# Kernel optimization log

Measured on AMD Instinct MI355X. Metric: run time of the kernel, lower is better.

## Reference

```python
import math
import jax, jax.numpy as jnp
import numpy as np

HID = 8
QNUM = 22
NUM_A = 11
NUM_LAYER = 6


def _ln(x, g, b, eps=1e-5):
    m = jnp.mean(x, axis=-1, keepdims=True)
    v = jnp.mean((x - m) ** 2, axis=-1, keepdims=True)
    return (x - m) / jnp.sqrt(v + eps) * g + b


def _conv1d_s2(x, w):
    # x: [N, C, L], w: [O, I, K=2], stride 2, no padding, no bias
    return jax.lax.conv_general_dilated(x, w, (2,), 'VALID', dimension_numbers=('NCH', 'OIH', 'NCH'))


def _qembed(hf):
    # product state amplitudes of RY(hf_q)|0> per qubit: [cos(t/2), sin(t/2)], kron over qubits
    c = jnp.cos(hf / 2.0)
    s = jnp.sin(hf / 2.0)
    state = jnp.ones((1,), dtype=hf.dtype)
    for q in range(hf.shape[0]):
        state = jnp.kron(state, jnp.stack([c[q], s[q]]))
    return state  # [2^Q]


def setup_inputs() -> dict:
    key = jax.random.key(0)
    ks = jax.random.split(key, 32)
    ix_list = [2] * NUM_A  # 2 electrons per atom -> n_e = 22 (even, <= QNUM)
    pos_ix = np.concatenate([np.arange(n) for n in ix_list])
    atom_ix = np.concatenate([np.full(n, i) for i, n in enumerate(ix_list)])
    L = NUM_LAYER
    g = lambda i, shp, s=1.0: jax.random.normal(ks[i], shp, dtype=jnp.float32) * s
    return dict(
        pos_a=g(0, (NUM_A, 3), 3.0),
        ix_a=jnp.asarray(ix_list, dtype=jnp.int32),
        pos_ix=jnp.asarray(pos_ix, dtype=jnp.int32),
        atom_ix=jnp.asarray(atom_ix, dtype=jnp.int32),
        rpos_w=g(1, (10, 3), 1.0),
        emb_w=g(2, (HID, 4), 0.5),
        emb_b=jnp.zeros((HID,), jnp.float32),
        Wq=g(3, (L, HID, HID), 0.35), bq=jnp.zeros((L, HID), jnp.float32),
        Wk=g(4, (L, HID, HID), 0.35), bk=jnp.zeros((L, HID), jnp.float32),
        Wv=g(5, (L, HID, HID), 0.35), bv=jnp.zeros((L, HID), jnp.float32),
        Wo=g(6, (L, HID, HID), 0.35), bo=jnp.zeros((L, HID), jnp.float32),
        W1=g(7, (L, 4 * HID, HID), 0.35), b1=jnp.zeros((L, 4 * HID), jnp.float32),
        W2=g(8, (L, HID, 4 * HID), 0.18), b2=jnp.zeros((L, HID), jnp.float32),
        ln1_g=jnp.ones((L, HID), jnp.float32), ln1_b=jnp.zeros((L, HID), jnp.float32),
        ln2_g=jnp.ones((L, HID), jnp.float32), ln2_b=jnp.zeros((L, HID), jnp.float32),
        Wi=g(9, (2 * HID, HID), 0.35), bi=jnp.zeros((2 * HID,), jnp.float32),
        ni_g=jnp.ones((2 * HID,), jnp.float32), ni_b=jnp.zeros((2 * HID,), jnp.float32),
        conv_a_w=g(10, (2 * HID, 2 * HID, 2), 0.25),
        conv_e_w=g(11, (2 * HID, 2 * HID, 2), 0.25),
        Wout=g(12, (2 ** QNUM, 2 * HID), 0.05),
        bout=jnp.zeros((2 ** QNUM,), jnp.float32),
    )


def reference(pos_a, ix_a, pos_ix, atom_ix, rpos_w, emb_w, emb_b,
              Wq, bq, Wk, bk, Wv, bv, Wo, bo, W1, b1, W2, b2,
              ln1_g, ln1_b, ln2_g, ln2_b,
              Wi, bi, ni_g, ni_b, conv_a_w, conv_e_w, Wout, bout):
    n_e = pos_ix.shape[0]
    pos_e = rpos_w[pos_ix] + pos_a[atom_ix]                 # [n_e, 3]
    ae = pos_e[:, None, :] - pos_a[None, :, :]              # [n_e, A, 3]
    r_ae = jnp.linalg.norm(ae, axis=2, keepdims=True)       # [n_e, A, 1]
    seq = jnp.concatenate([ae, r_ae], axis=-1) @ emb_w.T + emb_b  # [n_e, A, HID]
    amp_proto = ix_a.astype(seq.dtype)[None, :, None]       # broadcast of expanded ix_a
    amp_ae = jnp.std(r_ae, ddof=1)
    bias_ae = jnp.mean(r_ae)
    scale = jnp.sqrt(jnp.asarray(HID, seq.dtype))
    for l in range(Wq.shape[0]):
        x = amp_proto * seq
        q = x @ Wq[l].T + bq[l]
        k = x @ Wk[l].T + bk[l]
        v = x @ Wv[l].T + bv[l]
        att = jax.nn.softmax(jnp.einsum('bqh,bkh->bqk', q, k) / scale, axis=-1)
        a = jnp.einsum('bqk,bkh->bqh', att, v) @ Wo[l].T + bo[l]
        x = _ln(x + a, ln1_g[l], ln1_b[l])
        f = jax.nn.relu(x @ W1[l].T + b1[l]) @ W2[l].T + b2[l]
        seq = _ln(x + f, ln2_g[l], ln2_b[l])
    # pseudo-inverse projection (detached in torch)
    ae_inv = jax.lax.stop_gradient(jnp.linalg.inv(emb_w.T @ emb_w) @ emb_w.T)  # [4, HID]
    r = jnp.einsum('h,bah->ba', ae_inv[-1], seq)[..., None]  # [n_e, A, 1]
    r = amp_ae * (r - jnp.mean(r)) / jnp.std(r, ddof=1) + bias_ae
    x = (jnp.exp(-r) * amp_proto * seq) @ Wi.T + bi          # [n_e, A, 2*HID]
    x = jnp.swapaxes(x, -2, -1)                              # [n_e, 2*HID, A]
    y = jnp.mean(x, axis=-1)                                 # [n_e, 2*HID]
    amp_r = jnp.mean(jnp.exp(-jnp.swapaxes(r, -2, -1)), axis=-1)  # [n_e, 1]
    pad = jnp.zeros((x.shape[0], x.shape[1], 1), x.dtype)
    n_iter_a = (x.shape[-1] + 1) // 2
    for _ in range(n_iter_a):
        x = _conv1d_s2(jnp.concatenate([x, pad], axis=-1), conv_a_w)
    x = (amp_r * _ln(y + x[..., 0], ni_g, ni_b)).T           # [2*HID, n_e]
    y = jnp.mean(x, axis=-1)                                 # [2*HID]
    amp_r2 = jnp.mean(amp_r.T, axis=-1)                      # [1]
    x = x[None]                                              # [1, 2*HID, n_e]
    pad = jnp.zeros((1, x.shape[1], 1), x.dtype)
    n_iter_e = (x.shape[-1] + 1) // 2
    for _ in range(n_iter_e):
        x = _conv1d_s2(jnp.concatenate([x, pad], axis=-1), conv_e_w)
    x = amp_r2 * _ln(y + x[0, :, 0], ni_g, ni_b)             # [2*HID]
    psi = x @ Wout.T + bout                                  # [2^QNUM]
    hf = jnp.asarray(([math.pi, 0.0] * (n_e // 2)) + [0.0] * (QNUM - n_e), dtype=psi.dtype)
    bos = _qembed(hf)
    return psi + bos * (2.0 ** (QNUM / 2))
```

## Files before the change

kernel.cpp:

```cpp
#include <hip/hip_runtime.h>
#include <math.h>

#define NE 22
#define NA 11
#define HD 8
#define H2 16
#define QN 22
#define NL 6
#define CPAD 12
#define CSTR 17

struct QCS { float c[QN]; float s[QN]; };

#define RL(v, l) __uint_as_float(__builtin_amdgcn_readlane(__float_as_uint(v), (l)))

__device__ __forceinline__ float block_reduce_sum(float v, float* red, int tid) {
  red[tid] = v;
  __syncthreads();
  for (int off = 128; off > 0; off >>= 1) {
    if (tid < off) red[tid] += red[tid + off];
    __syncthreads();
  }
  float s = red[0];
  __syncthreads();
  return s;
}

__device__ __forceinline__ void ln_vec(const float* x, int n, const float* __restrict__ g,
                                       const float* __restrict__ bb, float* o) {
  float m = 0.f;
  for (int i = 0; i < n; i++) m += x[i];
  m /= (float)n;
  float v = 0.f;
  for (int i = 0; i < n; i++) { float d = x[i] - m; v += d * d; }
  v /= (float)n;
  float is = 1.0f / sqrtf(v + 1e-5f);
  for (int i = 0; i < n; i++) o[i] = (x[i] - m) * is * g[i] + bb[i];
}

__global__ __launch_bounds__(128, 1) void layers_kernel(
    const float* __restrict__ pos_a, const int* __restrict__ ix_a,
    const int* __restrict__ pos_ix, const int* __restrict__ atom_ix,
    const float* __restrict__ rpos_w, const float* __restrict__ emb_w,
    const float* __restrict__ emb_b,
    const float* __restrict__ Wq, const float* __restrict__ bq,
    const float* __restrict__ Wk, const float* __restrict__ bk,
    const float* __restrict__ Wv, const float* __restrict__ bv,
    const float* __restrict__ Wo, const float* __restrict__ bo,
    const float* __restrict__ W1, const float* __restrict__ b1,
    const float* __restrict__ W2, const float* __restrict__ b2,
    const float* __restrict__ ln1_g, const float* __restrict__ ln1_b,
    const float* __restrict__ ln2_g, const float* __restrict__ ln2_b,
    float* __restrict__ seq_out, float* __restrict__ rae_out)
{
  const int e = blockIdx.x;
  const int tid = threadIdx.x;
  const int a = tid >> 3;
  const int h = tid & 7;
  const bool act = (a < NA);

  __shared__ __align__(16) float sseq[NA][HD];
  __shared__ __align__(16) float sx[NA][HD];
  __shared__ __align__(16) float sq_[NA][HD];
  __shared__ __align__(16) float sk_[NA][HD];
  __shared__ __align__(16) float sv_[NA][HD];
  __shared__ __align__(16) float sav[NA][HD];
  __shared__ float ss[NA][12];
  __shared__ __align__(16) float sh_[NA][32];

  float amp_a = 0.f;
  if (act) {
    amp_a = (float)ix_a[a];
    int p = pos_ix[e], am = atom_ix[e];
    float d0 = rpos_w[p*3+0] + pos_a[am*3+0] - pos_a[a*3+0];
    float d1 = rpos_w[p*3+1] + pos_a[am*3+1] - pos_a[a*3+1];
    float d2 = rpos_w[p*3+2] + pos_a[am*3+2] - pos_a[a*3+2];
    float rae = sqrtf(d0*d0 + d1*d1 + d2*d2);
    float s = emb_b[h] + d0*emb_w[h*4+0] + d1*emb_w[h*4+1]
            + d2*emb_w[h*4+2] + rae*emb_w[h*4+3];
    sseq[a][h] = s;
    if (h == 0) rae_out[e*NA + a] = rae;
  }
  __syncthreads();

  const float iscale = 0.35355339059327373f;
  for (int l = 0; l < NL; l++) {
    float wq[8], wk[8], wv[8], wo[8], w1v[4][8], w2v[32];
    {
      const float4* q4 = (const float4*)(Wq + l*64 + h*8);
      float4 t0 = q4[0], t1 = q4[1];
      wq[0]=t0.x; wq[1]=t0.y; wq[2]=t0.z; wq[3]=t0.w; wq[4]=t1.x; wq[5]=t1.y; wq[6]=t1.z; wq[7]=t1.w;
      const float4* k4 = (const float4*)(Wk + l*64 + h*8);
      t0 = k4[0]; t1 = k4[1];
      wk[0]=t0.x; wk[1]=t0.y; wk[2]=t0.z; wk[3]=t0.w; wk[4]=t1.x; wk[5]=t1.y; wk[6]=t1.z; wk[7]=t1.w;
      const float4* v4 = (const float4*)(Wv + l*64 + h*8);
      t0 = v4[0]; t1 = v4[1];
      wv[0]=t0.x; wv[1]=t0.y; wv[2]=t0.z; wv[3]=t0.w; wv[4]=t1.x; wv[5]=t1.y; wv[6]=t1.z; wv[7]=t1.w;
      const float4* o4 = (const float4*)(Wo + l*64 + h*8);
      t0 = o4[0]; t1 = o4[1];
      wo[0]=t0.x; wo[1]=t0.y; wo[2]=t0.z; wo[3]=t0.w; wo[4]=t1.x; wo[5]=t1.y; wo[6]=t1.z; wo[7]=t1.w;
      #pragma unroll
      for (int j = 0; j < 4; j++) {
        const float4* w14 = (const float4*)(W1 + l*256 + (j*8 + h)*8);
        float4 u0 = w14[0], u1 = w14[1];
        w1v[j][0]=u0.x; w1v[j][1]=u0.y; w1v[j][2]=u0.z; w1v[j][3]=u0.w;
        w1v[j][4]=u1.x; w1v[j][5]=u1.y; w1v[j][6]=u1.z; w1v[j][7]=u1.w;
      }
      const float4* w24 = (const float4*)(W2 + l*256 + h*32);
      #pragma unroll
      for (int j = 0; j < 8; j++) {
        float4 u = w24[j];
        w2v[j*4+0]=u.x; w2v[j*4+1]=u.y; w2v[j*4+2]=u.z; w2v[j*4+3]=u.w;
      }
    }
    float bqv = bq[l*8+h], bkv = bk[l*8+h], bvv = bv[l*8+h], bov = bo[l*8+h];
    float b1v[4];
    #pragma unroll
    for (int j = 0; j < 4; j++) b1v[j] = b1[l*32 + j*8 + h];
    float b2v = b2[l*8+h];
    float g1 = ln1_g[l*8+h], be1 = ln1_b[l*8+h];
    float g2 = ln2_g[l*8+h], be2 = ln2_b[l*8+h];

    float xah = 0.f;
    if (act) { xah = amp_a * sseq[a][h]; sx[a][h] = xah; }
    __syncthreads();

    if (act) {
      float xr[8];
      float4 r0 = *(const float4*)&sx[a][0];
      float4 r1 = *(const float4*)&sx[a][4];
      xr[0]=r0.x; xr[1]=r0.y; xr[2]=r0.z; xr[3]=r0.w; xr[4]=r1.x; xr[5]=r1.y; xr[6]=r1.z; xr[7]=r1.w;
      float q_ = bqv, k_ = bkv, v_ = bvv;
      #pragma unroll
      for (int h2 = 0; h2 < 8; h2++) {
        q_ += xr[h2]*wq[h2];
        k_ += xr[h2]*wk[h2];
        v_ += xr[h2]*wv[h2];
      }
      sq_[a][h] = q_; sk_[a][h] = k_; sv_[a][h] = v_;
    }
    __syncthreads();

    if (act) {
      float4 q0 = *(const float4*)&sq_[a][0];
      float4 q1 = *(const float4*)&sq_[a][4];
      {
        int ka = h;
        float4 k0 = *(const float4*)&sk_[ka][0];
        float4 k1 = *(const float4*)&sk_[ka][4];
        ss[a][ka] = iscale * (q0.x*k0.x + q0.y*k0.y + q0.z*k0.z + q0.w*k0.w
                            + q1.x*k1.x + q1.y*k1.y + q1.z*k1.z + q1.w*k1.w);
      }
      if (h < 3) {
        int ka = 8 + h;
        float4 k0 = *(const float4*)&sk_[ka][0];
        float4 k1 = *(const float4*)&sk_[ka][4];
        ss[a][ka] = iscale * (q0.x*k0.x + q0.y*k0.y + q0.z*k0.z + q0.w*k0.w
                            + q1.x*k1.x + q1.y*k1.y + q1.z*k1.z + q1.w*k1.w);
      }
    }
    __syncthreads();

    float avh = 0.f;
    if (act) {
      float sc[NA], mx = -1e30f;
      #pragma unroll
      for (int ka = 0; ka < NA; ka++) { sc[ka] = ss[a][ka]; mx = fmaxf(mx, sc[ka]); }
      float den = 0.f;
      #pragma unroll
      for (int ka = 0; ka < NA; ka++) { sc[ka] = expf(sc[ka] - mx); den += sc[ka]; }
      float inv_den = 1.0f / den;
      #pragma unroll
      for (int ka = 0; ka < NA; ka++) avh += sc[ka] * sv_[ka][h];
      avh *= inv_den;
      sav[a][h] = avh;
    }
    __syncthreads();

    if (act) {
      float av[8];
      float4 r0 = *(const float4*)&sav[a][0];
      float4 r1 = *(const float4*)&sav[a][4];
      av[0]=r0.x; av[1]=r0.y; av[2]=r0.z; av[3]=r0.w; av[4]=r1.x; av[5]=r1.y; av[6]=r1.z; av[7]=r1.w;
      float t = bov;
      #pragma unroll
      for (int h2 = 0; h2 < 8; h2++) t += av[h2]*wo[h2];
      sq_[a][h] = xah + t;
    }
    __syncthreads();

    float xnh = 0.f;
    if (act) {
      float4 r0 = *(const float4*)&sq_[a][0];
      float4 r1 = *(const float4*)&sq_[a][4];
      float m = (r0.x+r0.y+r0.z+r0.w+r1.x+r1.y+r1.z+r1.w) * 0.125f;
      float d, v = 0.f;
      d=r0.x-m; v+=d*d; d=r0.y-m; v+=d*d; d=r0.z-m; v+=d*d; d=r0.w-m; v+=d*d;
      d=r1.x-m; v+=d*d; d=r1.y-m; v+=d*d; d=r1.z-m; v+=d*d; d=r1.w-m; v+=d*d;
      v *= 0.125f;
      float is = 1.0f / sqrtf(v + 1e-5f);
      float own = (h<4) ? (&r0.x)[h] : (&r1.x)[h-4];
      xnh = (own - m) * is * g1 + be1;
      sk_[a][h] = xnh;
    }
    __syncthreads();

    if (act) {
      float xn[8];
      float4 r0 = *(const float4*)&sk_[a][0];
      float4 r1 = *(const float4*)&sk_[a][4];
      xn[0]=r0.x; xn[1]=r0.y; xn[2]=r0.z; xn[3]=r0.w; xn[4]=r1.x; xn[5]=r1.y; xn[6]=r1.z; xn[7]=r1.w;
      #pragma unroll
      for (int j = 0; j < 4; j++) {
        float t = b1v[j];
        #pragma unroll
        for (int h2 = 0; h2 < 8; h2++) t += xn[h2]*w1v[j][h2];
        sh_[a][j*8+h] = fmaxf(t, 0.f);
      }
    }
    __syncthreads();

    if (act) {
      float f2 = b2v;
      #pragma unroll
      for (int j = 0; j < 8; j++) {
        float4 hv = *(const float4*)&sh_[a][j*4];
        f2 += hv.x*w2v[j*4+0] + hv.y*w2v[j*4+1] + hv.z*w2v[j*4+2] + hv.w*w2v[j*4+3];
      }
      sq_[a][h] = xnh + f2;
    }
    __syncthreads();

    if (act) {
      float4 r0 = *(const float4*)&sq_[a][0];
      float4 r1 = *(const float4*)&sq_[a][4];
      float m = (r0.x+r0.y+r0.z+r0.w+r1.x+r1.y+r1.z+r1.w) * 0.125f;
      float d, v = 0.f;
      d=r0.x-m; v+=d*d; d=r0.y-m; v+=d*d; d=r0.z-m; v+=d*d; d=r0.w-m; v+=d*d;
      d=r1.x-m; v+=d*d; d=r1.y-m; v+=d*d; d=r1.z-m; v+=d*d; d=r1.w-m; v+=d*d;
      v *= 0.125f;
      float is = 1.0f / sqrtf(v + 1e-5f);
      float own = (h<4) ? (&r0.x)[h] : (&r1.x)[h-4];
      sseq[a][h] = (own - m) * is * g2 + be2;
    }
    __syncthreads();
  }

  if (act) seq_out[e*NA*HD + a*HD + h] = sseq[a][h];
}

__global__ __launch_bounds__(256) void tail_kernel(
    const int* __restrict__ ix_a, const float* __restrict__ emb_w,
    const float* __restrict__ Wi, const float* __restrict__ bi,
    const float* __restrict__ ni_g, const float* __restrict__ ni_b,
    const float* __restrict__ conv_a_w, const float* __restrict__ conv_e_w,
    const float* __restrict__ seq_ws, const float* __restrict__ rae_ws,
    float* __restrict__ xf_out)
{
  const int tid = threadIdx.x;
  const int lane = tid & 63;
  const int b = tid / NA;
  const int a = tid % NA;
  const bool act = (tid < NE * NA);

  __shared__ __align__(16) float s_seq[NE][NA][HD];
  __shared__ float s_amp[NA];
  __shared__ float s_er[NE][NA];
  __shared__ float s_red[256];
  __shared__ float s_scal[8];
  __shared__ float s_aeinv[HD];
  __shared__ float convA[NE * CPAD * CSTR];
  __shared__ float convB[NE * CPAD * CSTR];
  __shared__ float s_y[NE][H2];
  __shared__ float s_ampr[NE];
  __shared__ float s_eA[24 * CSTR];
  __shared__ float s_eB[24 * CSTR];
  __shared__ float s_y2[H2];
  __shared__ float s_cewt[32 * H2];

  float cwr[8], wir[2];
  #pragma unroll
  for (int j = 0; j < 8; j++) cwr[j] = conv_a_w[j * 64 + lane];
  #pragma unroll
  for (int j = 0; j < 2; j++) wir[j] = Wi[j * 64 + lane];

  for (int s = tid; s < 512; s += 256) {
    int o = s >> 5, i = (s >> 1) & 15, k = s & 1;
    s_cewt[(i * 2 + k) * 16 + o] = conv_e_w[s];
  }
  for (int i = tid; i < NE*NA*HD/4; i += 256)
    ((float4*)s_seq)[i] = ((const float4*)seq_ws)[i];
  if (tid < NA) s_amp[tid] = (float)ix_a[tid];
  float rae = act ? rae_ws[tid] : 0.f;
  __syncthreads();

  {
    float sum = block_reduce_sum(act ? rae : 0.f, s_red, tid);
    float mean = sum / (float)(NE * NA);
    float d = act ? (rae - mean) : 0.f;
    float ss = block_reduce_sum(d * d, s_red, tid);
    if (tid == 0) { s_scal[0] = sqrtf(ss / (float)(NE * NA - 1)); s_scal[1] = mean; }
  }
  __syncthreads();

  if (tid == 0) {
    double M[4][8];
    for (int i = 0; i < 4; i++)
      for (int j = 0; j < 4; j++) {
        double s = 0.0;
        for (int h = 0; h < HD; h++) s += (double)emb_w[h * 4 + i] * (double)emb_w[h * 4 + j];
        M[i][j] = s;
        M[i][4 + j] = (i == j) ? 1.0 : 0.0;
      }
    for (int c = 0; c < 4; c++) {
      int piv = c;
      for (int r2 = c + 1; r2 < 4; r2++) if (fabs(M[r2][c]) > fabs(M[piv][c])) piv = r2;
      if (piv != c) for (int j = 0; j < 8; j++) { double t = M[c][j]; M[c][j] = M[piv][j]; M[piv][j] = t; }
      double dd = M[c][c];
      for (int j = 0; j < 8; j++) M[c][j] /= dd;
      for (int r2 = 0; r2 < 4; r2++) if (r2 != c) {
        double f = M[r2][c];
        for (int j = 0; j < 8; j++) M[r2][j] -= f * M[c][j];
      }
    }
    for (int h = 0; h < HD; h++) {
      double s = 0.0;
      for (int j = 0; j < 4; j++) s += M[3][4 + j] * (double)emb_w[h * 4 + j];
      s_aeinv[h] = (float)s;
    }
  }
  __syncthreads();

  float rv = 0.f;
  if (act) {
    #pragma unroll
    for (int h = 0; h < HD; h++) rv += s_aeinv[h] * s_seq[b][a][h];
  }
  {
    float sum = block_reduce_sum(act ? rv : 0.f, s_red, tid);
    float rm = sum / (float)(NE * NA);
    float d = act ? (rv - rm) : 0.f;
    float ss = block_reduce_sum(d * d, s_red, tid);
    float rs = sqrtf(ss / (float)(NE * NA - 1));
    if (act) {
      float rr = s_scal[0] * (rv - rm) / rs + s_scal[1];
      s_er[b][a] = expf(-rr);
    }
  }
  __syncthreads();

  if (act) {
    float e2 = s_er[b][a] * s_amp[a];
    float4 sq0 = *(const float4*)&s_seq[b][a][0];
    float4 sq1 = *(const float4*)&s_seq[b][a][4];
    float tv[HD] = { e2*sq0.x, e2*sq0.y, e2*sq0.z, e2*sq0.w,
                     e2*sq1.x, e2*sq1.y, e2*sq1.z, e2*sq1.w };
    #pragma unroll
    for (int o = 0; o < H2; o++) {
      float s = bi[o];
      #pragma unroll
      for (int h = 0; h < HD; h++) s += tv[h] * RL(wir[(o * 8 + h) >> 6], (o * 8 + h) & 63);
      convA[(b * CPAD + a) * CSTR + o] = s;
    }
  }
  for (int z = tid; z < NE * H2; z += 256)
    convA[((z >> 4) * CPAD + 11) * CSTR + (z & 15)] = 0.f;
  __syncthreads();

  for (int idx = tid; idx < NE * H2; idx += 256) {
    int bb = idx >> 4, o = idx & 15;
    float s = 0.f;
    for (int a2 = 0; a2 < NA; a2++) s += convA[(bb * CPAD + a2) * CSTR + o];
    s_y[bb][o] = s / (float)NA;
  }
  if (tid < NE) {
    float s = 0.f;
    for (int a2 = 0; a2 < NA; a2++) s += s_er[tid][a2];
    s_ampr[tid] = s / (float)NA;
  }
  __syncthreads();

  float* pin = convA;
  float* pout = convB;
  int L = NA;
  for (int it = 0; it < 6; it++) {
    int Lo = (L - 1) / 2 + 1;
    for (int pos = tid; pos < NE * Lo; pos += 256) {
      int bb = pos / Lo, j = pos - bb * Lo;
      const float* r0 = pin + (bb * CPAD + 2 * j) * CSTR;
      const float* r1 = r0 + CSTR;
      float x0[16], x1[16];
      #pragma unroll
      for (int i = 0; i < 16; i++) { x0[i] = r0[i]; x1[i] = r1[i]; }
      float* wrow = pout + (bb * CPAD + j) * CSTR;
      #pragma unroll
      for (int o = 0; o < 16; o++) {
        float acc = 0.f;
        #pragma unroll
        for (int i = 0; i < 16; i++) {
          acc += x0[i] * RL(cwr[((o * 16 + i) * 2) >> 6], ((o * 16 + i) * 2) & 63)
               + x1[i] * RL(cwr[((o * 16 + i) * 2 + 1) >> 6], ((o * 16 + i) * 2 + 1) & 63);
        }
        wrow[o] = acc;
      }
    }
    for (int z = tid; z < NE * H2; z += 256)
      pout[((z >> 4) * CPAD + Lo) * CSTR + (z & 15)] = 0.f;
    __syncthreads();
    float* t = pin; pin = pout; pout = t;
    L = Lo;
  }

  if (tid < NE) {
    float t[H2], oo[H2];
    #pragma unroll
    for (int o = 0; o < H2; o++) t[o] = s_y[tid][o] + pin[(tid * CPAD) * CSTR + o];
    ln_vec(t, H2, ni_g, ni_b, oo);
    float ar = s_ampr[tid];
    #pragma unroll
    for (int o = 0; o < H2; o++) s_eA[tid * CSTR + o] = ar * oo[o];
  }
  if (tid < H2) s_eA[NE * CSTR + tid] = 0.f;
  __syncthreads();
  if (tid < H2) {
    float s = 0.f;
    for (int bb = 0; bb < NE; bb++) s += s_eA[bb * CSTR + tid];
    s_y2[tid] = s / (float)NE;
  }
  if (tid == 0) {
    float s = 0.f;
    for (int bb = 0; bb < NE; bb++) s += s_ampr[bb];
    s_scal[4] = s / (float)NE;
  }
  __syncthreads();

  float* pinE = s_eA;
  float* poutE = s_eB;
  L = NE;
  for (int it = 0; it < 11; it++) {
    int Lo = (L - 1) / 2 + 1;
    for (int idx = tid; idx < Lo * H2; idx += 256) {
      int j = idx >> 4, o = idx & 15;
      const float* r0 = pinE + (2 * j) * CSTR;
      const float* r1 = r0 + CSTR;
      float acc = 0.f;
      #pragma unroll
      for (int i = 0; i < 16; i++)
        acc += r0[i] * s_cewt[(i * 2) * 16 + o] + r1[i] * s_cewt[(i * 2 + 1) * 16 + o];
      poutE[j * CSTR + o] = acc;
    }
    if (tid < H2) poutE[Lo * CSTR + tid] = 0.f;
    __syncthreads();
    float* t = pinE; pinE = poutE; poutE = t;
    L = Lo;
  }

  if (tid == 0) {
    float t[H2], oo[H2];
    for (int o = 0; o < H2; o++) t[o] = s_y2[o] + pinE[o];
    ln_vec(t, H2, ni_g, ni_b, oo);
    float a2 = s_scal[4];
    for (int o = 0; o < H2; o++) xf_out[o] = a2 * oo[o];
  }
}

__global__ __launch_bounds__(256) void psi_kernel(
    const float* __restrict__ Wout, const float* __restrict__ bout,
    const float* __restrict__ xf, float* __restrict__ out, QCS cs, int n)
{
  __shared__ float s_xf[H2];
  if (threadIdx.x < H2) s_xf[threadIdx.x] = xf[threadIdx.x];
  __syncthreads();
  int lane = threadIdx.x & 63;
  int waveBase = blockIdx.x * 256 + (threadIdx.x & ~63);
  if (waveBase >= n) return;
  const float4* W4 = (const float4*)Wout + (size_t)waveBase * 4;
  int q = lane & 3;
  float4 xq = make_float4(s_xf[q * 4], s_xf[q * 4 + 1], s_xf[q * 4 + 2], s_xf[q * 4 + 3]);
  #pragma unroll
  for (int j = 0; j < 4; j++) {
    float4 w = W4[j * 64 + lane];
    float p = w.x * xq.x + w.y * xq.y + w.z * xq.z + w.w * xq.w;
    p += __shfl_xor(p, 1, 64);
    p += __shfl_xor(p, 2, 64);
    if (q == 0) {
      int row = waveBase + j * 16 + (lane >> 2);
      float acc = bout[row] + p;
      unsigned int ii = (unsigned int)row;
      float pr = (float)(1 << (QN / 2));
      #pragma unroll
      for (int qb = 0; qb < QN; qb++)
        pr *= ((ii >> (QN - 1 - qb)) & 1u) ? cs.s[qb] : cs.c[qb];
      out[row] = acc + pr;
    }
  }
}

extern "C" void kernel_launch(void* const* d_in, const int* in_sizes, int n_in,
                              void* d_out, int out_size, void* d_ws, size_t ws_size,
                              hipStream_t stream) {
  const float* pos_a   = (const float*)d_in[0];
  const int*   ix_a    = (const int*)d_in[1];
  const int*   pos_ix  = (const int*)d_in[2];
  const int*   atom_ix = (const int*)d_in[3];
  const float* rpos_w  = (const float*)d_in[4];
  const float* emb_w   = (const float*)d_in[5];
  const float* emb_b   = (const float*)d_in[6];
  const float* Wq = (const float*)d_in[7];   const float* bq = (const float*)d_in[8];
  const float* Wk = (const float*)d_in[9];   const float* bk = (const float*)d_in[10];
  const float* Wv = (const float*)d_in[11];  const float* bv = (const float*)d_in[12];
  const float* Wo = (const float*)d_in[13];  const float* bo = (const float*)d_in[14];
  const float* W1 = (const float*)d_in[15];  const float* b1 = (const float*)d_in[16];
  const float* W2 = (const float*)d_in[17];  const float* b2 = (const float*)d_in[18];
  const float* ln1_g = (const float*)d_in[19]; const float* ln1_b = (const float*)d_in[20];
  const float* ln2_g = (const float*)d_in[21]; const float* ln2_b = (const float*)d_in[22];
  const float* Wi = (const float*)d_in[23];  const float* bi = (const float*)d_in[24];
  const float* ni_g = (const float*)d_in[25]; const float* ni_b = (const float*)d_in[26];
  const float* conv_a_w = (const float*)d_in[27];
  const float* conv_e_w = (const float*)d_in[28];
  const float* Wout = (const float*)d_in[29];
  const float* bout = (const float*)d_in[30];

  float* ws = (float*)d_ws;
  float* xf      = ws;
  float* seq_ws  = ws + 64;
  float* rae_ws  = ws + 64 + NE*NA*HD;

  layers_kernel<<<NE, 128, 0, stream>>>(pos_a, ix_a, pos_ix, atom_ix, rpos_w,
      emb_w, emb_b, Wq, bq, Wk, bk, Wv, bv, Wo, bo, W1, b1, W2, b2,
      ln1_g, ln1_b, ln2_g, ln2_b, seq_ws, rae_ws);

  tail_kernel<<<1, 256, 0, stream>>>(ix_a, emb_w, Wi, bi, ni_g, ni_b,
      conv_a_w, conv_e_w, seq_ws, rae_ws, xf);

  QCS cs;
  int n_e = in_sizes[2];
  for (int q = 0; q < QN; q++) {
    float hf = (q < n_e && (q % 2 == 0)) ? (float)M_PI : 0.0f;
    cs.c[q] = cosf(0.5f * hf);
    cs.s[q] = sinf(0.5f * hf);
  }

  int n = out_size;
  int blocks = (n + 255) / 256;
  psi_kernel<<<blocks, 256, 0, stream>>>(Wout, bout, xf, (float*)d_out, cs, n);
}
```

Baseline: 483.6 us.

## Fuse layers and tail kernels via last-block atomic counter; closed-form 4x4 inverse

```diff
diff --git a/kernel.cpp b/kernel.cpp
--- a/kernel.cpp
+++ b/kernel.cpp
@@ -26,19 +26,29 @@
   return s;
 }
 
-__device__ __forceinline__ void ln_vec(const float* x, int n, const float* __restrict__ g,
-                                       const float* __restrict__ bb, float* o) {
+template<int N>
+__device__ __forceinline__ void ln_t(const float* x, const float* __restrict__ g,
+                                     const float* __restrict__ bb, float* o) {
   float m = 0.f;
-  for (int i = 0; i < n; i++) m += x[i];
-  m /= (float)n;
+  #pragma unroll
+  for (int i = 0; i < N; i++) m += x[i];
+  m *= (1.0f / (float)N);
   float v = 0.f;
-  for (int i = 0; i < n; i++) { float d = x[i] - m; v += d * d; }
-  v /= (float)n;
+  #pragma unroll
+  for (int i = 0; i < N; i++) { float d = x[i] - m; v += d * d; }
+  v *= (1.0f / (float)N);
   float is = 1.0f / sqrtf(v + 1e-5f);
-  for (int i = 0; i < n; i++) o[i] = (x[i] - m) * is * g[i] + bb[i];
+  #pragma unroll
+  for (int i = 0; i < N; i++) o[i] = (x[i] - m) * is * g[i] + bb[i];
 }
 
-__global__ __launch_bounds__(128, 1) void layers_kernel(
+__device__ __forceinline__ double det3(double a, double b, double c,
+                                       double d, double e, double f,
+                                       double g, double h, double i) {
+  return a * (e * i - f * h) - b * (d * i - f * g) + c * (d * h - e * g);
+}
+
+__global__ __launch_bounds__(256) void net_kernel(
     const float* __restrict__ pos_a, const int* __restrict__ ix_a,
     const int* __restrict__ pos_ix, const int* __restrict__ atom_ix,
     const float* __restrict__ rpos_w, const float* __restrict__ emb_w,
@@ -51,7 +61,11 @@
     const float* __restrict__ W2, const float* __restrict__ b2,
     const float* __restrict__ ln1_g, const float* __restrict__ ln1_b,
     const float* __restrict__ ln2_g, const float* __restrict__ ln2_b,
-    float* __restrict__ seq_out, float* __restrict__ rae_out)
+    const float* __restrict__ Wi, const float* __restrict__ bi,
+    const float* __restrict__ ni_g, const float* __restrict__ ni_b,
+    const float* __restrict__ conv_a_w, const float* __restrict__ conv_e_w,
+    float* __restrict__ seq_ws, float* __restrict__ rae_ws,
+    int* __restrict__ counter, float* __restrict__ xf_out)
 {
   const int e = blockIdx.x;
   const int tid = threadIdx.x;
@@ -67,6 +81,7 @@
   __shared__ __align__(16) float sav[NA][HD];
   __shared__ float ss[NA][12];
   __shared__ __align__(16) float sh_[NA][32];
+  __shared__ int s_win;
 
   float amp_a = 0.f;
   if (act) {
@@ -79,14 +94,15 @@
     float s = emb_b[h] + d0*emb_w[h*4+0] + d1*emb_w[h*4+1]
             + d2*emb_w[h*4+2] + rae*emb_w[h*4+3];
     sseq[a][h] = s;
-    if (h == 0) rae_out[e*NA + a] = rae;
+    if (h == 0) rae_ws[e*NA + a] = rae;
   }
   __syncthreads();
 
   const float iscale = 0.35355339059327373f;
   for (int l = 0; l < NL; l++) {
     float wq[8], wk[8], wv[8], wo[8], w1v[4][8], w2v[32];
-    {
+    float bqv=0, bkv=0, bvv=0, bov=0, b1v[4]={0,0,0,0}, b2v=0, g1=0, be1=0, g2=0, be2=0;
+    if (act) {
       const float4* q4 = (const float4*)(Wq + l*64 + h*8);
       float4 t0 = q4[0], t1 = q4[1];
       wq[0]=t0.x; wq[1]=t0.y; wq[2]=t0.z; wq[3]=t0.w; wq[4]=t1.x; wq[5]=t1.y; wq[6]=t1.z; wq[7]=t1.w;
@@ -112,24 +128,22 @@
         float4 u = w24[j];
         w2v[j*4+0]=u.x; w2v[j*4+1]=u.y; w2v[j*4+2]=u.z; w2v[j*4+3]=u.w;
       }
-    }
-    float bqv = bq[l*8+h], bkv = bk[l*8+h], bvv = bv[l*8+h], bov = bo[l*8+h];
-    float b1v[4];
-    #pragma unroll
-    for (int j = 0; j < 4; j++) b1v[j] = b1[l*32 + j*8 + h];
-    float b2v = b2[l*8+h];
-    float g1 = ln1_g[l*8+h], be1 = ln1_b[l*8+h];
-    float g2 = ln2_g[l*8+h], be2 = ln2_b[l*8+h];
+      bqv = bq[l*8+h]; bkv = bk[l*8+h]; bvv = bv[l*8+h]; bov = bo[l*8+h];
+      #pragma unroll
+      for (int j = 0; j < 4; j++) b1v[j] = b1[l*32 + j*8 + h];
+      b2v = b2[l*8+h];
+      g1 = ln1_g[l*8+h]; be1 = ln1_b[l*8+h];
+      g2 = ln2_g[l*8+h]; be2 = ln2_b[l*8+h];
+    }
 
     float xah = 0.f;
     if (act) { xah = amp_a * sseq[a][h]; sx[a][h] = xah; }
     __syncthreads();
 
     if (act) {
-      float xr[8];
       float4 r0 = *(const float4*)&sx[a][0];
       float4 r1 = *(const float4*)&sx[a][4];
-      xr[0]=r0.x; xr[1]=r0.y; xr[2]=r0.z; xr[3]=r0.w; xr[4]=r1.x; xr[5]=r1.y; xr[6]=r1.z; xr[7]=r1.w;
+      float xr[8] = { r0.x, r0.y, r0.z, r0.w, r1.x, r1.y, r1.z, r1.w };
       float q_ = bqv, k_ = bkv, v_ = bvv;
       #pragma unroll
       for (int h2 = 0; h2 < 8; h2++) {
@@ -161,7 +175,6 @@
     }
     __syncthreads();
 
-    float avh = 0.f;
     if (act) {
       float sc[NA], mx = -1e30f;
       #pragma unroll
@@ -170,22 +183,23 @@
       #pragma unroll
       for (int ka = 0; ka < NA; ka++) { sc[ka] = expf(sc[ka] - mx); den += sc[ka]; }
       float inv_den = 1.0f / den;
+      float avh = 0.f;
       #pragma unroll
       for (int ka = 0; ka < NA; ka++) avh += sc[ka] * sv_[ka][h];
-      avh *= inv_den;
-      sav[a][h] = avh;
-    }
-    __syncthreads();
-
-    if (act) {
-      float av[8];
+      sav[a][h] = avh * inv_den;
+    }
+    __syncthreads();
+
+    float xr_own = 0.f;
+    if (act) {
       float4 r0 = *(const float4*)&sav[a][0];
       float4 r1 = *(const float4*)&sav[a][4];
-      av[0]=r0.x; av[1]=r0.y; av[2]=r0.z; av[3]=r0.w; av[4]=r1.x; av[5]=r1.y; av[6]=r1.z; av[7]=r1.w;
+      float av[8] = { r0.x, r0.y, r0.z, r0.w, r1.x, r1.y, r1.z, r1.w };
       float t = bov;
       #pragma unroll
       for (int h2 = 0; h2 < 8; h2++) t += av[h2]*wo[h2];
-      sq_[a][h] = xah + t;
+      xr_own = xah + t;
+      sq_[a][h] = xr_own;
     }
     __syncthreads();
 
@@ -199,17 +213,15 @@
       d=r1.x-m; v+=d*d; d=r1.y-m; v+=d*d; d=r1.z-m; v+=d*d; d=r1.w-m; v+=d*d;
       v *= 0.125f;
       float is = 1.0f / sqrtf(v + 1e-5f);
-      float own = (h<4) ? (&r0.x)[h] : (&r1.x)[h-4];
-      xnh = (own - m) * is * g1 + be1;
+      xnh = (xr_own - m) * is * g1 + be1;
       sk_[a][h] = xnh;
     }
     __syncthreads();
 
     if (act) {
-      float xn[8];
       float4 r0 = *(const float4*)&sk_[a][0];
       float4 r1 = *(const float4*)&sk_[a][4];
-      xn[0]=r0.x; xn[1]=r0.y; xn[2]=r0.z; xn[3]=r0.w; xn[4]=r1.x; xn[5]=r1.y; xn[6]=r1.z; xn[7]=r1.w;
+      float xn[8] = { r0.x, r0.y, r0.z, r0.w, r1.x, r1.y, r1.z, r1.w };
       #pragma unroll
       for (int j = 0; j < 4; j++) {
         float t = b1v[j];
@@ -220,6 +232,7 @@
     }
     __syncthreads();
 
+    float xr2_own = 0.f;
     if (act) {
       float f2 = b2v;
       #pragma unroll
@@ -227,7 +240,8 @@
         float4 hv = *(const float4*)&sh_[a][j*4];
         f2 += hv.x*w2v[j*4+0] + hv.y*w2v[j*4+1] + hv.z*w2v[j*4+2] + hv.w*w2v[j*4+3];
       }
-      sq_[a][h] = xnh + f2;
+      xr2_own = xnh + f2;
+      sq_[a][h] = xr2_own;
     }
     __syncthreads();
 
@@ -240,28 +254,24 @@
       d=r1.x-m; v+=d*d; d=r1.y-m; v+=d*d; d=r1.z-m; v+=d*d; d=r1.w-m; v+=d*d;
       v *= 0.125f;
       float is = 1.0f / sqrtf(v + 1e-5f);
-      float own = (h<4) ? (&r0.x)[h] : (&r1.x)[h-4];
-      sseq[a][h] = (own - m) * is * g2 + be2;
-    }
-    __syncthreads();
-  }
-
-  if (act) seq_out[e*NA*HD + a*HD + h] = sseq[a][h];
-}
-
-__global__ __launch_bounds__(256) void tail_kernel(
-    const int* __restrict__ ix_a, const float* __restrict__ emb_w,
-    const float* __restrict__ Wi, const float* __restrict__ bi,
-    const float* __restrict__ ni_g, const float* __restrict__ ni_b,
-    const float* __restrict__ conv_a_w, const float* __restrict__ conv_e_w,
-    const float* __restrict__ seq_ws, const float* __restrict__ rae_ws,
-    float* __restrict__ xf_out)
-{
-  const int tid = threadIdx.x;
+      sseq[a][h] = (xr2_own - m) * is * g2 + be2;
+    }
+    __syncthreads();
+
+  }
+
+  if (act) seq_ws[e*NA*HD + a*HD + h] = sseq[a][h];
+
+  __threadfence();
+  if (tid == 0) s_win = (atomicAdd(counter, 1) == NE - 1) ? 1 : 0;
+  __syncthreads();
+  if (!s_win) return;
+  __threadfence();
+
   const int lane = tid & 63;
   const int b = tid / NA;
-  const int a = tid % NA;
-  const bool act = (tid < NE * NA);
+  const int a2i = tid % NA;
+  const bool act2 = (tid < NE * NA);
 
   __shared__ __align__(16) float s_seq[NE][NA][HD];
   __shared__ float s_amp[NA];
@@ -291,76 +301,74 @@
   for (int i = tid; i < NE*NA*HD/4; i += 256)
     ((float4*)s_seq)[i] = ((const float4*)seq_ws)[i];
   if (tid < NA) s_amp[tid] = (float)ix_a[tid];
-  float rae = act ? rae_ws[tid] : 0.f;
+  float rae2 = act2 ? rae_ws[tid] : 0.f;
   __syncthreads();
 
   {
-    float sum = block_reduce_sum(act ? rae : 0.f, s_red, tid);
+    float sum = block_reduce_sum(act2 ? rae2 : 0.f, s_red, tid);
     float mean = sum / (float)(NE * NA);
-    float d = act ? (rae - mean) : 0.f;
-    float ss = block_reduce_sum(d * d, s_red, tid);
-    if (tid == 0) { s_scal[0] = sqrtf(ss / (float)(NE * NA - 1)); s_scal[1] = mean; }
+    float d = act2 ? (rae2 - mean) : 0.f;
+    float ssum = block_reduce_sum(d * d, s_red, tid);
+    if (tid == 0) { s_scal[0] = sqrtf(ssum / (float)(NE * NA - 1)); s_scal[1] = mean; }
   }
   __syncthreads();
 
   if (tid == 0) {
-    double M[4][8];
+    float ew[32];
+    #pragma unroll
+    for (int i = 0; i < 32; i++) ew[i] = emb_w[i];
+    double m[4][4];
+    #pragma unroll
     for (int i = 0; i < 4; i++)
+      #pragma unroll
       for (int j = 0; j < 4; j++) {
         double s = 0.0;
-        for (int h = 0; h < HD; h++) s += (double)emb_w[h * 4 + i] * (double)emb_w[h * 4 + j];
-        M[i][j] = s;
-        M[i][4 + j] = (i == j) ? 1.0 : 0.0;
-      }
-    for (int c = 0; c < 4; c++) {
-      int piv = c;
-      for (int r2 = c + 1; r2 < 4; r2++) if (fabs(M[r2][c]) > fabs(M[piv][c])) piv = r2;
-      if (piv != c) for (int j = 0; j < 8; j++) { double t = M[c][j]; M[c][j] = M[piv][j]; M[piv][j] = t; }
-      double dd = M[c][c];
-      for (int j = 0; j < 8; j++) M[c][j] /= dd;
-      for (int r2 = 0; r2 < 4; r2++) if (r2 != c) {
-        double f = M[r2][c];
-        for (int j = 0; j < 8; j++) M[r2][j] -= f * M[c][j];
-      }
-    }
-    for (int h = 0; h < HD; h++) {
-      double s = 0.0;
-      for (int j = 0; j < 4; j++) s += M[3][4 + j] * (double)emb_w[h * 4 + j];
-      s_aeinv[h] = (float)s;
-    }
+        #pragma unroll
+        for (int hh = 0; hh < HD; hh++) s += (double)ew[hh*4+i] * (double)ew[hh*4+j];
+        m[i][j] = s;
+      }
+    double mn0 = det3(m[0][1],m[0][2],m[0][3], m[1][1],m[1][2],m[1][3], m[2][1],m[2][2],m[2][3]);
+    double mn1 = det3(m[0][0],m[0][2],m[0][3], m[1][0],m[1][2],m[1][3], m[2][0],m[2][2],m[2][3]);
+    double mn2 = det3(m[0][0],m[0][1],m[0][3], m[1][0],m[1][1],m[1][3], m[2][0],m[2][1],m[2][3]);
+    double mn3 = det3(m[0][0],m[0][1],m[0][2], m[1][0],m[1][1],m[1][2], m[2][0],m[2][1],m[2][2]);
+    double det = -m[3][0]*mn0 + m[3][1]*mn1 - m[3][2]*mn2 + m[3][3]*mn3;
+    double y0 = -mn0/det, y1 = mn1/det, y2 = -mn2/det, y3 = mn3/det;
+    #pragma unroll
+    for (int hh = 0; hh < HD; hh++)
+      s_aeinv[hh] = (float)(y0*ew[hh*4+0] + y1*ew[hh*4+1] + y2*ew[hh*4+2] + y3*ew[hh*4+3]);
   }
   __syncthreads();
 
   float rv = 0.f;
-  if (act) {
-    #pragma unroll
-    for (int h = 0; h < HD; h++) rv += s_aeinv[h] * s_seq[b][a][h];
+  if (act2) {
+    #pragma unroll
+    for (int hh = 0; hh < HD; hh++) rv += s_aeinv[hh] * s_seq[b][a2i][hh];
   }
   {
-    float sum = block_reduce_sum(act ? rv : 0.f, s_red, tid);
+    float sum = block_reduce_sum(act2 ? rv : 0.f, s_red, tid);
     float rm = sum / (float)(NE * NA);
-    float d = act ? (rv - rm) : 0.f;
-    float ss = block_reduce_sum(d * d, s_red, tid);
-    float rs = sqrtf(ss / (float)(NE * NA - 1));
-    if (act) {
+    float d = act2 ? (rv - rm) : 0.f;
+    float ssum = block_reduce_sum(d * d, s_red, tid);
+    float rs = sqrtf(ssum / (float)(NE * NA - 1));
+    if (act2) {
       float rr = s_scal[0] * (rv - rm) / rs + s_scal[1];
-      s_er[b][a] = expf(-rr);
-    }
-  }
-  __syncthreads();
-
-  if (act) {
-    float e2 = s_er[b][a] * s_amp[a];
-    float4 sq0 = *(const float4*)&s_seq[b][a][0];
-    float4 sq1 = *(const float4*)&s_seq[b][a][4];
+      s_er[b][a2i] = expf(-rr);
+    }
+  }
+  __syncthreads();
+
+  if (act2) {
+    float e2 = s_er[b][a2i] * s_amp[a2i];
+    float4 sq0 = *(const float4*)&s_seq[b][a2i][0];
+    float4 sq1 = *(const float4*)&s_seq[b][a2i][4];
     float tv[HD] = { e2*sq0.x, e2*sq0.y, e2*sq0.z, e2*sq0.w,
                      e2*sq1.x, e2*sq1.y, e2*sq1.z, e2*sq1.w };
     #pragma unroll
     for (int o = 0; o < H2; o++) {
       float s = bi[o];
       #pragma unroll
-      for (int h = 0; h < HD; h++) s += tv[h] * RL(wir[(o * 8 + h) >> 6], (o * 8 + h) & 63);
-      convA[(b * CPAD + a) * CSTR + o] = s;
+      for (int hh = 0; hh < HD; hh++) s += tv[hh] * RL(wir[(o * 8 + hh) >> 6], (o * 8 + hh) & 63);
+      convA[(b * CPAD + a2i) * CSTR + o] = s;
     }
   }
   for (int z = tid; z < NE * H2; z += 256)
@@ -370,12 +378,12 @@
   for (int idx = tid; idx < NE * H2; idx += 256) {
     int bb = idx >> 4, o = idx & 15;
     float s = 0.f;
-    for (int a2 = 0; a2 < NA; a2++) s += convA[(bb * CPAD + a2) * CSTR + o];
+    for (int aa = 0; aa < NA; aa++) s += convA[(bb * CPAD + aa) * CSTR + o];
     s_y[bb][o] = s / (float)NA;
   }
   if (tid < NE) {
     float s = 0.f;
-    for (int a2 = 0; a2 < NA; a2++) s += s_er[tid][a2];
+    for (int aa = 0; aa < NA; aa++) s += s_er[tid][aa];
     s_ampr[tid] = s / (float)NA;
   }
   __syncthreads();
@@ -415,7 +423,7 @@
     float t[H2], oo[H2];
     #pragma unroll
     for (int o = 0; o < H2; o++) t[o] = s_y[tid][o] + pin[(tid * CPAD) * CSTR + o];
-    ln_vec(t, H2, ni_g, ni_b, oo);
+    ln_t<H2>(t, ni_g, ni_b, oo);
     float ar = s_ampr[tid];
     #pragma unroll
     for (int o = 0; o < H2; o++) s_eA[tid * CSTR + o] = ar * oo[o];
@@ -457,9 +465,11 @@
 
   if (tid == 0) {
     float t[H2], oo[H2];
+    #pragma unroll
     for (int o = 0; o < H2; o++) t[o] = s_y2[o] + pinE[o];
-    ln_vec(t, H2, ni_g, ni_b, oo);
+    ln_t<H2>(t, ni_g, ni_b, oo);
     float a2 = s_scal[4];
+    #pragma unroll
     for (int o = 0; o < H2; o++) xf_out[o] = a2 * oo[o];
   }
 }
@@ -523,15 +533,16 @@
 
   float* ws = (float*)d_ws;
   float* xf      = ws;
+  int*   counter = (int*)(ws + 32);
   float* seq_ws  = ws + 64;
   float* rae_ws  = ws + 64 + NE*NA*HD;
 
-  layers_kernel<<<NE, 128, 0, stream>>>(pos_a, ix_a, pos_ix, atom_ix, rpos_w,
+  hipMemsetAsync(counter, 0, sizeof(int), stream);
+
+  net_kernel<<<NE, 256, 0, stream>>>(pos_a, ix_a, pos_ix, atom_ix, rpos_w,
       emb_w, emb_b, Wq, bq, Wk, bk, Wv, bv, Wo, bo, W1, b1, W2, b2,
-      ln1_g, ln1_b, ln2_g, ln2_b, seq_ws, rae_ws);
-
-  tail_kernel<<<1, 256, 0, stream>>>(ix_a, emb_w, Wi, bi, ni_g, ni_b,
-      conv_a_w, conv_e_w, seq_ws, rae_ws, xf);
+      ln1_g, ln1_b, ln2_g, ln2_b, Wi, bi, ni_g, ni_b, conv_a_w, conv_e_w,
+      seq_ws, rae_ws, counter, xf);
 
   QCS cs;
   int n_e = in_sizes[2];
```

After: 483.8 us. About the same (+0.0%).
